# Performance work log

Hardware: AMD Instinct MI355X
Metric: run time of the kernel (lower is better)

Reference implementation:

```python
import jax, jax.numpy as jnp
import numpy as np

D_MODEL = 1024
OMEGA_DIM = 64
VQ_CODES = 256
VQ_DIM = 64
N_PARAMS = OMEGA_DIM * (OMEGA_DIM - 1) // 2  # 2016
TRIU_R, TRIU_C = np.triu_indices(OMEGA_DIM, k=1)
RMS_EPS = 1e-6
NORM_EPS = 1e-12  # F.normalize default


def setup_inputs() -> dict:
    key = jax.random.key(0)
    ks = jax.random.split(key, 12)
    B, L = 16, 4096
    s = 0.02
    return {
        "x": jax.random.normal(ks[0], (B, L, D_MODEL), jnp.float32),
        "omega_proj_w": jax.random.normal(ks[1], (N_PARAMS, D_MODEL), jnp.float32) * s,
        "omega_proj_b": jnp.zeros((N_PARAMS,), jnp.float32),
        "omega_out_w": jax.random.normal(ks[2], (D_MODEL, OMEGA_DIM), jnp.float32) * s,
        "omega_out_b": jnp.zeros((D_MODEL,), jnp.float32),
        "vq_proj_in_w": jax.random.normal(ks[3], (VQ_DIM, D_MODEL), jnp.float32) * s,
        "vq_proj_in_b": jnp.zeros((VQ_DIM,), jnp.float32),
        "vq_proj_out_w": jax.random.normal(ks[4], (D_MODEL, VQ_DIM), jnp.float32) * s,
        "vq_proj_out_b": jnp.zeros((D_MODEL,), jnp.float32),
        "codebook": jax.random.normal(ks[5], (VQ_CODES, VQ_DIM), jnp.float32),
        "omega_mix": jnp.float32(0.1),
        "vq_mix": jnp.float32(0.05),
        "norm_w": jnp.ones((D_MODEL,), jnp.float32),
    }


def _normalize(v):
    n = jnp.linalg.norm(v, axis=-1, keepdims=True)
    return v / jnp.maximum(n, NORM_EPS)


def _rmsnorm(x, w):
    ms = jnp.mean(x * x, axis=-1, keepdims=True)
    return x * jax.lax.rsqrt(ms + RMS_EPS) * w


def reference(x, omega_proj_w, omega_proj_b, omega_out_w, omega_out_b,
              vq_proj_in_w, vq_proj_in_b, vq_proj_out_w, vq_proj_out_b,
              codebook, omega_mix, vq_mix, norm_w):
    B = x.shape[0]
    residual = x
    h_mean = jnp.mean(x, axis=1)  # [B, d_model]

    # --- Lie branch: skew-symmetric Omega -> Cayley (3rd-order Neumann) ---
    params = h_mean @ omega_proj_w.T + omega_proj_b  # [B, n_params]
    omega = jnp.zeros((B, OMEGA_DIM, OMEGA_DIM), x.dtype).at[:, TRIU_R, TRIU_C].set(params)
    omega = omega - jnp.swapaxes(omega, -1, -2)
    I = jnp.eye(OMEGA_DIM, dtype=x.dtype)
    omega2 = jnp.einsum('bij,bjk->bik', omega, omega)
    omega3 = jnp.einsum('bij,bjk->bik', omega2, omega)
    G = I + omega + 0.5 * omega2 + (1.0 / 6.0) * omega3  # [B, n, n]

    x_head = x[:, :, :OMEGA_DIM]
    x_rotated = jnp.einsum('bld,bde->ble', x_head, G)
    lie_out = x_rotated @ omega_out_w.T + omega_out_b  # [B, L, d_model]

    # --- VQ branch: cosine-sim codebook lookup with straight-through ---
    vq_input = h_mean @ vq_proj_in_w.T + vq_proj_in_b  # [B, vq_dim]
    scores = _normalize(vq_input) @ _normalize(codebook).T  # [B, vq_codes]
    vq_idx = jnp.argmax(scores, axis=-1)
    vq_code = codebook[vq_idx]  # [B, vq_dim]
    vq_out = vq_input + jax.lax.stop_gradient(vq_code - vq_input)
    vq_contribution = (vq_out @ vq_proj_out_w.T + vq_proj_out_b)[:, None, :]  # [B,1,d_model]

    out = residual + omega_mix * lie_out + vq_mix * vq_contribution
    return _rmsnorm(out, norm_w)
```

## Files before the change

### kernel.cpp

```cpp
#include <hip/hip_runtime.h>
#include <hip/hip_bf16.h>
#include <math.h>

#define BB 16
#define LL 4096
#define DD 1024
#define OD 64
#define NP 2016
#define NC 256
#define VD 64
#define NCHUNK 64
#define LCH (LL / NCHUNK)
#define TT 16
#define TPB 256
#define NROW (NP + VD)

typedef __attribute__((ext_vector_type(8))) short bf16x8;
typedef __attribute__((ext_vector_type(4))) float f32x4;

__device__ __forceinline__ int triu_idx(int r, int c) {
  return r * 63 - (r * (r - 1)) / 2 + (c - r - 1);
}

__device__ __forceinline__ unsigned short f2bf(float f) {
  unsigned int u = __float_as_uint(f);
  u += 0x7fffu + ((u >> 16) & 1u);
  return (unsigned short)(u >> 16);
}

__global__ void k_partial(const float* __restrict__ x, float* __restrict__ partial) {
  const int b = blockIdx.y, ch = blockIdx.x, tid = threadIdx.x;
  const float4* xp = (const float4*)(x + ((size_t)b * LL + (size_t)ch * LCH) * DD) + tid;
  float4 s = make_float4(0.f, 0.f, 0.f, 0.f);
  #pragma unroll 8
  for (int l = 0; l < LCH; ++l) {
    float4 v = xp[(size_t)l * (DD / 4)];
    s.x += v.x; s.y += v.y; s.z += v.z; s.w += v.w;
  }
  ((float4*)(partial + ((size_t)(b * NCHUNK + ch)) * DD))[tid] = s;
}

__global__ void k_mean(const float* __restrict__ partial, float* __restrict__ hm) {
  const int b = blockIdx.x, tid = threadIdx.x;
  float4 s = make_float4(0.f, 0.f, 0.f, 0.f);
  for (int c = 0; c < NCHUNK; ++c) {
    float4 v = ((const float4*)(partial + ((size_t)(b * NCHUNK + c)) * DD))[tid];
    s.x += v.x; s.y += v.y; s.z += v.z; s.w += v.w;
  }
  const float inv = 1.0f / (float)LL;
  s.x *= inv; s.y *= inv; s.z *= inv; s.w *= inv;
  ((float4*)(hm + (size_t)b * DD))[tid] = s;
}

__global__ void k_params(const float* __restrict__ hm,
                         const float* __restrict__ opw, const float* __restrict__ opb,
                         const float* __restrict__ viw, const float* __restrict__ vib,
                         float* __restrict__ params, float* __restrict__ vqi_g) {
  const int wave = threadIdx.x >> 6, lane = threadIdx.x & 63;
  const int p = blockIdx.x * 4 + wave;
  if (p >= NROW) return;
  const bool isvq = (p >= NP);
  const float* wr = isvq ? (viw + (size_t)(p - NP) * DD) : (opw + (size_t)p * DD);
  float acc[BB];
  #pragma unroll
  for (int b = 0; b < BB; ++b) acc[b] = 0.f;
  for (int i = 0; i < DD; i += 64) {
    const float wv = wr[i + lane];
    #pragma unroll
    for (int b = 0; b < BB; ++b) acc[b] = fmaf(wv, hm[b * DD + i + lane], acc[b]);
  }
  const float bias = isvq ? vib[p - NP] : opb[p];
  #pragma unroll
  for (int b = 0; b < BB; ++b) {
    float v = acc[b];
    #pragma unroll
    for (int mk = 32; mk; mk >>= 1) v += __shfl_xor(v, mk, 64);
    if (lane == 0) {
      if (isvq) vqi_g[(size_t)b * VD + (p - NP)] = v + bias;
      else      params[(size_t)b * NP + p] = v + bias;
    }
  }
}

__global__ void k_perb(const float* __restrict__ params, const float* __restrict__ vqi_g,
                       const float* __restrict__ cb,
                       const float* __restrict__ oob, const float* __restrict__ vow,
                       const float* __restrict__ vob,
                       const float* __restrict__ omix_p, const float* __restrict__ vmix_p,
                       float* __restrict__ Gout, float* __restrict__ cvec) {
  const int b = blockIdx.x, tid = threadIdx.x;
  __shared__ float om[OD][OD + 1];
  __shared__ float om2[OD][OD + 1];
  __shared__ float vqi[VD];
  __shared__ float sc[NC];
  __shared__ int si[NC];
  __shared__ float cd[VD];
  __shared__ float nv_s;
  const float* par = params + (size_t)b * NP;

  if (tid < VD) vqi[tid] = vqi_g[(size_t)b * VD + tid];
  for (int e2 = tid; e2 < OD * OD; e2 += 256) {
    int i = e2 >> 6, j = e2 & 63;
    float v = 0.f;
    if (i < j) v = par[triu_idx(i, j)];
    else if (i > j) v = -par[triu_idx(j, i)];
    om[i][j] = v;
  }
  __syncthreads();
  if (tid == 0) {
    float s = 0.f;
    for (int k = 0; k < VD; ++k) s += vqi[k] * vqi[k];
    nv_s = fmaxf(sqrtf(s), 1e-12f);
  }
  for (int e2 = tid; e2 < OD * OD; e2 += 256) {
    int i = e2 >> 6, j = e2 & 63;
    float s = 0.f;
    #pragma unroll 8
    for (int k = 0; k < OD; ++k) s = fmaf(om[i][k], om[k][j], s);
    om2[i][j] = s;
  }
  __syncthreads();
  for (int e2 = tid; e2 < OD * OD; e2 += 256) {
    int i = e2 >> 6, j = e2 & 63;
    float s3 = 0.f;
    #pragma unroll 8
    for (int k = 0; k < OD; ++k) s3 = fmaf(om2[i][k], om[k][j], s3);
    float gv = om[i][j] + 0.5f * om2[i][j] + (1.f / 6.f) * s3 + (i == j ? 1.f : 0.f);
    Gout[(size_t)b * OD * OD + e2] = gv;
  }
  {
    const float* cr = cb + (size_t)tid * VD;
    float dot = 0.f, ssq = 0.f;
    #pragma unroll 8
    for (int k = 0; k < VD; ++k) { float cvv = cr[k]; dot = fmaf(cvv, vqi[k], dot); ssq = fmaf(cvv, cvv, ssq); }
    float ncn = fmaxf(sqrtf(ssq), 1e-12f);
    sc[tid] = dot / (nv_s * ncn);
    si[tid] = tid;
  }
  __syncthreads();
  for (int s = 128; s > 0; s >>= 1) {
    if (tid < s) {
      float a = sc[tid], b2 = sc[tid + s];
      int ia = si[tid], ib = si[tid + s];
      if (b2 > a || (b2 == a && ib < ia)) { sc[tid] = b2; si[tid] = ib; }
    }
    __syncthreads();
  }
  const int best = si[0];
  if (tid < VD) cd[tid] = cb[(size_t)best * VD + tid];
  __syncthreads();
  const float omix = omix_p[0], vmix = vmix_p[0];
  for (int e = tid; e < DD; e += 256) {
    float a = vob[e];
    const float* wr = vow + (size_t)e * VD;
    #pragma unroll 8
    for (int k = 0; k < VD; ++k) a = fmaf(cd[k], wr[k], a);
    cvec[(size_t)b * DD + e] = fmaf(omix, oob[e], vmix * a);
  }
}

__global__ void k_MTB(const float* __restrict__ G, const float* __restrict__ oow,
                      const float* __restrict__ omix_p, unsigned short* __restrict__ MTB) {
  const int b = blockIdx.y, eb = blockIdx.x * 64, tid = threadIdx.x;
  __shared__ float g[OD][OD + 1];
  __shared__ float wl[64][65];
  for (int e2 = tid; e2 < OD * OD; e2 += 256) g[e2 >> 6][e2 & 63] = G[(size_t)b * OD * OD + e2];
  for (int e2 = tid; e2 < 64 * 64; e2 += 256) wl[e2 >> 6][e2 & 63] = oow[(size_t)(eb + (e2 >> 6)) * 64 + (e2 & 63)];
  __syncthreads();
  const float omix = omix_p[0];
  for (int o = tid; o < 4096; o += 256) {
    int el = o >> 6, d = o & 63;
    float s = 0.f;
    #pragma unroll
    for (int k = 0; k < 64; ++k) s = fmaf(g[d][k], wl[el][k], s);
    MTB[((size_t)b * DD + eb + el) * OD + d] = f2bf(omix * s);
  }
}

#define STAGE_XH(BUF, TTOK)                                                          \
  if (stager) {                                                                      \
    const float4 v = *(const float4*)(x + xrow + (size_t)((TTOK) + stok) * DD + sd0);\
    unsigned int lo = (unsigned int)f2bf(v.x) | ((unsigned int)f2bf(v.y) << 16);     \
    unsigned int hi = (unsigned int)f2bf(v.z) | ((unsigned int)f2bf(v.w) << 16);     \
    *(uint2*)((char*)&(BUF)[0][0] + stok * 144 + sd0 * 2) = make_uint2(lo, hi);      \
  }

#define LOAD_RES(DST, TTOK)                                                          \
  _Pragma("unroll")                                                                  \
  for (int et = 0; et < 4; ++et) {                                                   \
    _Pragma("unroll")                                                                \
    for (int r = 0; r < 4; ++r)                                                      \
      DST[et][r] = x[xrow + (size_t)((TTOK) + g * 4 + r) * DD + ebase + et * 16 + c];\
  }

#define COMPUTE_TILE(XBUF, RES, PAR, TTOK)                                           \
  {                                                                                  \
    const char* xbB = (const char*)&(XBUF)[0][0];                                    \
    bf16x8 af0 = *(const bf16x8*)(xbB + c * 144 + 0 * 64 + g * 16);                  \
    bf16x8 af1 = *(const bf16x8*)(xbB + c * 144 + 1 * 64 + g * 16);                  \
    f32x4 acc[4];                                                                    \
    _Pragma("unroll")                                                                \
    for (int et = 0; et < 4; ++et) {                                                 \
      acc[et] = (f32x4){0.f, 0.f, 0.f, 0.f};                                         \
      acc[et] = __builtin_amdgcn_mfma_f32_16x16x32_bf16(af0, bf[et][0], acc[et], 0, 0, 0); \
      acc[et] = __builtin_amdgcn_mfma_f32_16x16x32_bf16(af1, bf[et][1], acc[et], 0, 0, 0); \
    }                                                                                \
    float p[4] = {0.f, 0.f, 0.f, 0.f};                                               \
    _Pragma("unroll")                                                                \
    for (int et = 0; et < 4; ++et) {                                                 \
      _Pragma("unroll")                                                              \
      for (int r = 0; r < 4; ++r) {                                                  \
        const float y = RES[et][r] + acc[et][r] + ce_r[et];                          \
        acc[et][r] = y;                                                              \
        p[r] = fmaf(y, y, p[r]);                                                     \
      }                                                                              \
    }                                                                                \
    _Pragma("unroll")                                                                \
    for (int mk = 1; mk < 16; mk <<= 1) {                                            \
      _Pragma("unroll")                                                              \
      for (int r = 0; r < 4; ++r) p[r] += __shfl_xor(p[r], mk, 64);                  \
    }                                                                                \
    if (c == 0) {                                                                    \
      _Pragma("unroll")                                                              \
      for (int r = 0; r < 4; ++r) red[PAR][g * 4 + r][w] = p[r];                     \
    }                                                                                \
    __syncthreads();                                                                 \
    float sc_r[4];                                                                   \
    _Pragma("unroll")                                                                \
    for (int r = 0; r < 4; ++r) {                                                    \
      const float4* rp = (const float4*)&red[PAR][g * 4 + r][0];                     \
      const float4 s0 = rp[0], s1 = rp[1], s2 = rp[2], s3 = rp[3];                   \
      const float s = s0.x + s0.y + s0.z + s0.w + s1.x + s1.y + s1.z + s1.w          \
                    + s2.x + s2.y + s2.z + s2.w + s3.x + s3.y + s3.z + s3.w;         \
      sc_r[r] = rsqrtf(s * (1.f / (float)DD) + 1e-6f);                               \
    }                                                                                \
    _Pragma("unroll")                                                                \
    for (int et = 0; et < 4; ++et) {                                                 \
      _Pragma("unroll")                                                              \
      for (int r = 0; r < 4; ++r) {                                                  \
        out[xrow + (size_t)((TTOK) + g * 4 + r) * DD + ebase + et * 16 + c] =        \
            acc[et][r] * sc_r[r] * nw_r[et];                                         \
      }                                                                              \
    }                                                                                \
  }

__global__ __launch_bounds__(1024)
void k_mfma(const float* __restrict__ x, const unsigned short* __restrict__ MTB,
            const float* __restrict__ cvec, const float* __restrict__ nw,
            float* __restrict__ out) {
  const int b = blockIdx.y;
  const int Tblk = blockIdx.x * TPB;
  const int tid = threadIdx.x;
  const int w = tid >> 6, lane = tid & 63;
  const int c = lane & 15, g = lane >> 4;
  const int ebase = w * 64;

  __shared__ unsigned short xh[2][TT][72];
  __shared__ float red[2][TT][20];

  bf16x8 bf[4][2];
  {
    const unsigned short* mp = MTB + ((size_t)b * DD + ebase + c) * OD + g * 8;
    #pragma unroll
    for (int et = 0; et < 4; ++et) {
      #pragma unroll
      for (int ks = 0; ks < 2; ++ks)
        bf[et][ks] = *(const bf16x8*)(mp + (size_t)et * 16 * OD + ks * 32);
    }
  }
  float ce_r[4], nw_r[4];
  #pragma unroll
  for (int et = 0; et < 4; ++et) {
    ce_r[et] = cvec[(size_t)b * DD + ebase + et * 16 + c];
    nw_r[et] = nw[ebase + et * 16 + c];
  }

  const size_t xrow = ((size_t)b * LL + Tblk) * DD;
  const int stok = tid >> 4, sd0 = (tid & 15) * 4;
  const bool stager = (tid < 256);

  float resA[4][4], resB[4][4];

  STAGE_XH(xh[0], 0)
  LOAD_RES(resA, 0)
  __syncthreads();

  #pragma unroll 1
  for (int it = 0; it < TPB / (2 * TT); ++it) {
    const int te = it * 2 * TT;
    const int to = te + TT;
    const int tn = te + 2 * TT;
    STAGE_XH(xh[1], to)
    LOAD_RES(resB, to)
    COMPUTE_TILE(xh[0], resA, 0, te)
    if (it + 1 < TPB / (2 * TT)) {
      STAGE_XH(xh[0], tn)
      LOAD_RES(resA, tn)
    }
    COMPUTE_TILE(xh[1], resB, 1, to)
  }
}

extern "C" void kernel_launch(void* const* d_in, const int* in_sizes, int n_in,
                              void* d_out, int out_size, void* d_ws, size_t ws_size,
                              hipStream_t stream) {
  (void)in_sizes; (void)n_in; (void)out_size; (void)ws_size;
  const float* x    = (const float*)d_in[0];
  const float* opw  = (const float*)d_in[1];
  const float* opb  = (const float*)d_in[2];
  const float* oow  = (const float*)d_in[3];
  const float* oob  = (const float*)d_in[4];
  const float* viw  = (const float*)d_in[5];
  const float* vib  = (const float*)d_in[6];
  const float* vow  = (const float*)d_in[7];
  const float* vob  = (const float*)d_in[8];
  const float* cb   = (const float*)d_in[9];
  const float* omix = (const float*)d_in[10];
  const float* vmix = (const float*)d_in[11];
  const float* nw   = (const float*)d_in[12];
  float* out = (float*)d_out;

  float* ws      = (float*)d_ws;
  float* partial = ws;
  float* hm      = ws + 1048576;
  float* params  = ws + 1064960;
  float* vqi_g   = ws + 1097216;
  float* G       = ws + 1098240;
  unsigned short* MTB = (unsigned short*)(ws + 1163776);
  float* cvec    = ws + 1688064;

  k_partial<<<dim3(NCHUNK, BB), 256, 0, stream>>>(x, partial);
  k_mean<<<BB, 256, 0, stream>>>(partial, hm);
  k_params<<<NROW / 4, 256, 0, stream>>>(hm, opw, opb, viw, vib, params, vqi_g);
  k_perb<<<BB, 256, 0, stream>>>(params, vqi_g, cb, oob, vow, vob, omix, vmix, G, cvec);
  k_MTB<<<dim3(16, BB), 256, 0, stream>>>(G, oow, omix, MTB);
  k_mfma<<<dim3(LL / TPB, BB), 1024, 0, stream>>>(x, MTB, cvec, nw, out);
}
```

Before: 252.3 us.

## Fuse all six stages into one persistent kernel with grid barriers

Merges the mean reduction, parameter GEMV, Cayley/VQ per-batch work, MTB build and the MFMA main pass into one 256-block persistent kernel. Stages are separated by atomic-counter grid barriers, and the counters are reset with a memset before each launch. The G matrix is no longer written to global memory: each block recomputes G for its batch in shared memory before forming its slice of MTB. This removes five launch gaps and the small-grid serial stages. The risks are deadlock if all 256 blocks of 1024 threads are not co-resident, the cost of redundant G computation, and lower parallelism in the reduction stages.

```diff
diff --git a/kernel.cpp b/kernel.cpp
--- a/kernel.cpp
+++ b/kernel.cpp
@@ -9,11 +9,10 @@
 #define NP 2016
 #define NC 256
 #define VD 64
-#define NCHUNK 64
-#define LCH (LL / NCHUNK)
 #define TT 16
 #define TPB 256
 #define NROW (NP + VD)
+#define NBLK 256
 
 typedef __attribute__((ext_vector_type(8))) short bf16x8;
 typedef __attribute__((ext_vector_type(4))) float f32x4;
@@ -21,283 +20,297 @@
 __device__ __forceinline__ int triu_idx(int r, int c) {
   return r * 63 - (r * (r - 1)) / 2 + (c - r - 1);
 }
-
 __device__ __forceinline__ unsigned short f2bf(float f) {
   unsigned int u = __float_as_uint(f);
   u += 0x7fffu + ((u >> 16) & 1u);
   return (unsigned short)(u >> 16);
 }
 
-__global__ void k_partial(const float* __restrict__ x, float* __restrict__ partial) {
-  const int b = blockIdx.y, ch = blockIdx.x, tid = threadIdx.x;
-  const float4* xp = (const float4*)(x + ((size_t)b * LL + (size_t)ch * LCH) * DD) + tid;
-  float4 s = make_float4(0.f, 0.f, 0.f, 0.f);
-  #pragma unroll 8
-  for (int l = 0; l < LCH; ++l) {
-    float4 v = xp[(size_t)l * (DD / 4)];
-    s.x += v.x; s.y += v.y; s.z += v.z; s.w += v.w;
-  }
-  ((float4*)(partial + ((size_t)(b * NCHUNK + ch)) * DD))[tid] = s;
-}
-
-__global__ void k_mean(const float* __restrict__ partial, float* __restrict__ hm) {
-  const int b = blockIdx.x, tid = threadIdx.x;
-  float4 s = make_float4(0.f, 0.f, 0.f, 0.f);
-  for (int c = 0; c < NCHUNK; ++c) {
-    float4 v = ((const float4*)(partial + ((size_t)(b * NCHUNK + c)) * DD))[tid];
-    s.x += v.x; s.y += v.y; s.z += v.z; s.w += v.w;
-  }
-  const float inv = 1.0f / (float)LL;
-  s.x *= inv; s.y *= inv; s.z *= inv; s.w *= inv;
-  ((float4*)(hm + (size_t)b * DD))[tid] = s;
-}
-
-__global__ void k_params(const float* __restrict__ hm,
-                         const float* __restrict__ opw, const float* __restrict__ opb,
-                         const float* __restrict__ viw, const float* __restrict__ vib,
-                         float* __restrict__ params, float* __restrict__ vqi_g) {
-  const int wave = threadIdx.x >> 6, lane = threadIdx.x & 63;
-  const int p = blockIdx.x * 4 + wave;
-  if (p >= NROW) return;
-  const bool isvq = (p >= NP);
-  const float* wr = isvq ? (viw + (size_t)(p - NP) * DD) : (opw + (size_t)p * DD);
-  float acc[BB];
-  #pragma unroll
-  for (int b = 0; b < BB; ++b) acc[b] = 0.f;
-  for (int i = 0; i < DD; i += 64) {
-    const float wv = wr[i + lane];
+__device__ __forceinline__ void gbar(unsigned int* cnt) {
+  __syncthreads();
+  __threadfence();
+  if (threadIdx.x == 0) {
+    atomicAdd(cnt, 1u);
+    while (atomicAdd(cnt, 0u) < NBLK) __builtin_amdgcn_s_sleep(2);
+  }
+  __syncthreads();
+  __threadfence();
+}
+
+__global__ __launch_bounds__(1024)
+void k_mega(const float* __restrict__ x,
+            const float* __restrict__ opw, const float* __restrict__ opb,
+            const float* __restrict__ oow, const float* __restrict__ oob,
+            const float* __restrict__ viw, const float* __restrict__ vib,
+            const float* __restrict__ vow, const float* __restrict__ vob,
+            const float* __restrict__ cb,
+            const float* __restrict__ omix_p, const float* __restrict__ vmix_p,
+            const float* __restrict__ nw,
+            float* __restrict__ partial2, float* __restrict__ hm,
+            float* __restrict__ params, float* __restrict__ vqi_g,
+            unsigned short* __restrict__ MTB, float* __restrict__ cvec,
+            unsigned int* cnt, float* __restrict__ out) {
+  const int bid = blockIdx.x, tid = threadIdx.x;
+  __shared__ __align__(16) char smem[49920];
+
+  {
+    const int b = bid >> 4, seg = bid & 15;
+    const int c4 = tid & 255, toff = tid >> 8;
+    const float4* xp = (const float4*)(x + ((size_t)b * LL + seg * 256 + toff) * DD) + c4;
+    float4 s = make_float4(0.f, 0.f, 0.f, 0.f);
+    #pragma unroll 8
+    for (int l = 0; l < 64; ++l) {
+      float4 v = xp[(size_t)l * DD];
+      s.x += v.x; s.y += v.y; s.z += v.z; s.w += v.w;
+    }
+    ((float4*)(partial2 + (size_t)(bid * 4 + toff) * DD))[c4] = s;
+  }
+  gbar(cnt + 0);
+
+  if (bid < BB) {
+    float s = 0.f;
+    const float* pr = partial2 + (size_t)bid * 64 * DD + tid;
+    #pragma unroll 8
+    for (int r2 = 0; r2 < 64; ++r2) s += pr[(size_t)r2 * DD];
+    hm[(size_t)bid * DD + tid] = s * (1.f / (float)LL);
+  }
+  gbar(cnt + 1);
+
+  {
+    const int w = tid >> 6, lane = tid & 63;
+    const int p = bid * 16 + w;
+    if (p < NROW) {
+      const bool isvq = (p >= NP);
+      const float* wr = isvq ? (viw + (size_t)(p - NP) * DD) : (opw + (size_t)p * DD);
+      float acc[BB];
+      #pragma unroll
+      for (int b = 0; b < BB; ++b) acc[b] = 0.f;
+      for (int i = 0; i < DD; i += 64) {
+        const float wv = wr[i + lane];
+        #pragma unroll
+        for (int b = 0; b < BB; ++b) acc[b] = fmaf(wv, hm[b * DD + i + lane], acc[b]);
+      }
+      const float bias = isvq ? vib[p - NP] : opb[p];
+      #pragma unroll
+      for (int b = 0; b < BB; ++b) {
+        float v = acc[b];
+        #pragma unroll
+        for (int mk = 32; mk; mk >>= 1) v += __shfl_xor(v, mk, 64);
+        if (lane == 0) {
+          if (isvq) vqi_g[(size_t)b * VD + (p - NP)] = v + bias;
+          else      params[(size_t)b * NP + p] = v + bias;
+        }
+      }
+    }
+  }
+  gbar(cnt + 2);
+
+  {
+    const int b = bid >> 4, chunk = bid & 15, eb = chunk * 64;
+    float (*om)[OD + 1]  = (float(*)[OD + 1])(smem);
+    float (*om2)[OD + 1] = (float(*)[OD + 1])(smem + 16640);
+    float (*gs)[OD + 1]  = (float(*)[OD + 1])(smem + 33280);
+    const float* par = params + (size_t)b * NP;
+    const float omix = omix_p[0];
+
+    for (int e2 = tid; e2 < OD * OD; e2 += 1024) {
+      int i = e2 >> 6, j = e2 & 63;
+      float v = 0.f;
+      if (i < j) v = par[triu_idx(i, j)];
+      else if (i > j) v = -par[triu_idx(j, i)];
+      om[i][j] = v;
+    }
+    __syncthreads();
+    for (int e2 = tid; e2 < OD * OD; e2 += 1024) {
+      int i = e2 >> 6, j = e2 & 63;
+      float s = 0.f;
+      #pragma unroll 8
+      for (int k = 0; k < OD; ++k) s = fmaf(om[i][k], om[k][j], s);
+      om2[i][j] = s;
+    }
+    __syncthreads();
+    for (int e2 = tid; e2 < OD * OD; e2 += 1024) {
+      int i = e2 >> 6, j = e2 & 63;
+      float s3 = 0.f;
+      #pragma unroll 8
+      for (int k = 0; k < OD; ++k) s3 = fmaf(om2[i][k], om[k][j], s3);
+      gs[i][j] = om[i][j] + 0.5f * om2[i][j] + (1.f / 6.f) * s3 + (i == j ? 1.f : 0.f);
+    }
+    __syncthreads();
+    float (*wl)[OD + 1] = (float(*)[OD + 1])(smem);
+    for (int e2 = tid; e2 < 64 * 64; e2 += 1024)
+      wl[e2 >> 6][e2 & 63] = oow[(size_t)(eb + (e2 >> 6)) * 64 + (e2 & 63)];
+    __syncthreads();
+    for (int o = tid; o < 4096; o += 1024) {
+      int el = o >> 6, d = o & 63;
+      float s = 0.f;
+      #pragma unroll
+      for (int k = 0; k < 64; ++k) s = fmaf(gs[d][k], wl[el][k], s);
+      MTB[((size_t)b * DD + eb + el) * OD + d] = f2bf(omix * s);
+    }
+    if (chunk == 0) {
+      float* vq  = (float*)(smem + 16640);
+      float* scb = (float*)(smem + 16640 + 256);
+      int*   sib = (int*)  (smem + 16640 + 1280);
+      float* cd  = (float*)(smem + 16640 + 2304);
+      float* nvp = (float*)(smem + 16640 + 2560);
+      if (tid < VD) vq[tid] = vqi_g[(size_t)b * VD + tid];
+      __syncthreads();
+      if (tid == 0) {
+        float s = 0.f;
+        for (int k = 0; k < VD; ++k) s += vq[k] * vq[k];
+        nvp[0] = fmaxf(sqrtf(s), 1e-12f);
+      }
+      __syncthreads();
+      if (tid < NC) {
+        const float* cr = cb + (size_t)tid * VD;
+        float dot = 0.f, ssq = 0.f;
+        #pragma unroll 8
+        for (int k = 0; k < VD; ++k) { float cv = cr[k]; dot = fmaf(cv, vq[k], dot); ssq = fmaf(cv, cv, ssq); }
+        scb[tid] = dot / (nvp[0] * fmaxf(sqrtf(ssq), 1e-12f));
+        sib[tid] = tid;
+      }
+      __syncthreads();
+      for (int s2 = 128; s2 > 0; s2 >>= 1) {
+        if (tid < s2) {
+          float a = scb[tid], b2 = scb[tid + s2];
+          int ia = sib[tid], ib = sib[tid + s2];
+          if (b2 > a || (b2 == a && ib < ia)) { scb[tid] = b2; sib[tid] = ib; }
+        }
+        __syncthreads();
+      }
+      const int best = sib[0];
+      if (tid < VD) cd[tid] = cb[(size_t)best * VD + tid];
+      __syncthreads();
+      const float vmix = vmix_p[0];
+      {
+        const int e = tid;
+        float a = vob[e];
+        const float* wr2 = vow + (size_t)e * VD;
+        #pragma unroll 8
+        for (int k = 0; k < VD; ++k) a = fmaf(cd[k], wr2[k], a);
+        cvec[(size_t)b * DD + e] = fmaf(omix, oob[e], vmix * a);
+      }
+    }
+  }
+  gbar(cnt + 3);
+
+  {
+    const int b = bid >> 4;
+    const int Tblk = (bid & 15) * TPB;
+    const int w = tid >> 6, lane = tid & 63;
+    const int c = lane & 15, g = lane >> 4;
+    const int ebase = w * 64;
+
+#define XB(q) ((char*)smem + (q) * 2304)
+#define RB(q) ((char*)smem + 4608 + (q) * 1280)
+
+    bf16x8 bf[4][2];
+    {
+      const unsigned short* mp = MTB + ((size_t)b * DD + ebase + c) * OD + g * 8;
+      #pragma unroll
+      for (int et = 0; et < 4; ++et) {
+        #pragma unroll
+        for (int ks = 0; ks < 2; ++ks)
+          bf[et][ks] = *(const bf16x8*)(mp + (size_t)et * 16 * OD + ks * 32);
+      }
+    }
+    float ce_r[4], nw_r[4];
     #pragma unroll
-    for (int b = 0; b < BB; ++b) acc[b] = fmaf(wv, hm[b * DD + i + lane], acc[b]);
-  }
-  const float bias = isvq ? vib[p - NP] : opb[p];
-  #pragma unroll
-  for (int b = 0; b < BB; ++b) {
-    float v = acc[b];
-    #pragma unroll
-    for (int mk = 32; mk; mk >>= 1) v += __shfl_xor(v, mk, 64);
-    if (lane == 0) {
-      if (isvq) vqi_g[(size_t)b * VD + (p - NP)] = v + bias;
-      else      params[(size_t)b * NP + p] = v + bias;
-    }
-  }
-}
-
-__global__ void k_perb(const float* __restrict__ params, const float* __restrict__ vqi_g,
-                       const float* __restrict__ cb,
-                       const float* __restrict__ oob, const float* __restrict__ vow,
-                       const float* __restrict__ vob,
-                       const float* __restrict__ omix_p, const float* __restrict__ vmix_p,
-                       float* __restrict__ Gout, float* __restrict__ cvec) {
-  const int b = blockIdx.x, tid = threadIdx.x;
-  __shared__ float om[OD][OD + 1];
-  __shared__ float om2[OD][OD + 1];
-  __shared__ float vqi[VD];
-  __shared__ float sc[NC];
-  __shared__ int si[NC];
-  __shared__ float cd[VD];
-  __shared__ float nv_s;
-  const float* par = params + (size_t)b * NP;
-
-  if (tid < VD) vqi[tid] = vqi_g[(size_t)b * VD + tid];
-  for (int e2 = tid; e2 < OD * OD; e2 += 256) {
-    int i = e2 >> 6, j = e2 & 63;
-    float v = 0.f;
-    if (i < j) v = par[triu_idx(i, j)];
-    else if (i > j) v = -par[triu_idx(j, i)];
-    om[i][j] = v;
-  }
-  __syncthreads();
-  if (tid == 0) {
-    float s = 0.f;
-    for (int k = 0; k < VD; ++k) s += vqi[k] * vqi[k];
-    nv_s = fmaxf(sqrtf(s), 1e-12f);
-  }
-  for (int e2 = tid; e2 < OD * OD; e2 += 256) {
-    int i = e2 >> 6, j = e2 & 63;
-    float s = 0.f;
-    #pragma unroll 8
-    for (int k = 0; k < OD; ++k) s = fmaf(om[i][k], om[k][j], s);
-    om2[i][j] = s;
-  }
-  __syncthreads();
-  for (int e2 = tid; e2 < OD * OD; e2 += 256) {
-    int i = e2 >> 6, j = e2 & 63;
-    float s3 = 0.f;
-    #pragma unroll 8
-    for (int k = 0; k < OD; ++k) s3 = fmaf(om2[i][k], om[k][j], s3);
-    float gv = om[i][j] + 0.5f * om2[i][j] + (1.f / 6.f) * s3 + (i == j ? 1.f : 0.f);
-    Gout[(size_t)b * OD * OD + e2] = gv;
-  }
-  {
-    const float* cr = cb + (size_t)tid * VD;
-    float dot = 0.f, ssq = 0.f;
-    #pragma unroll 8
-    for (int k = 0; k < VD; ++k) { float cvv = cr[k]; dot = fmaf(cvv, vqi[k], dot); ssq = fmaf(cvv, cvv, ssq); }
-    float ncn = fmaxf(sqrtf(ssq), 1e-12f);
-    sc[tid] = dot / (nv_s * ncn);
-    si[tid] = tid;
-  }
-  __syncthreads();
-  for (int s = 128; s > 0; s >>= 1) {
-    if (tid < s) {
-      float a = sc[tid], b2 = sc[tid + s];
-      int ia = si[tid], ib = si[tid + s];
-      if (b2 > a || (b2 == a && ib < ia)) { sc[tid] = b2; si[tid] = ib; }
-    }
-    __syncthreads();
-  }
-  const int best = si[0];
-  if (tid < VD) cd[tid] = cb[(size_t)best * VD + tid];
-  __syncthreads();
-  const float omix = omix_p[0], vmix = vmix_p[0];
-  for (int e = tid; e < DD; e += 256) {
-    float a = vob[e];
-    const float* wr = vow + (size_t)e * VD;
-    #pragma unroll 8
-    for (int k = 0; k < VD; ++k) a = fmaf(cd[k], wr[k], a);
-    cvec[(size_t)b * DD + e] = fmaf(omix, oob[e], vmix * a);
-  }
-}
-
-__global__ void k_MTB(const float* __restrict__ G, const float* __restrict__ oow,
-                      const float* __restrict__ omix_p, unsigned short* __restrict__ MTB) {
-  const int b = blockIdx.y, eb = blockIdx.x * 64, tid = threadIdx.x;
-  __shared__ float g[OD][OD + 1];
-  __shared__ float wl[64][65];
-  for (int e2 = tid; e2 < OD * OD; e2 += 256) g[e2 >> 6][e2 & 63] = G[(size_t)b * OD * OD + e2];
-  for (int e2 = tid; e2 < 64 * 64; e2 += 256) wl[e2 >> 6][e2 & 63] = oow[(size_t)(eb + (e2 >> 6)) * 64 + (e2 & 63)];
-  __syncthreads();
-  const float omix = omix_p[0];
-  for (int o = tid; o < 4096; o += 256) {
-    int el = o >> 6, d = o & 63;
-    float s = 0.f;
-    #pragma unroll
-    for (int k = 0; k < 64; ++k) s = fmaf(g[d][k], wl[el][k], s);
-    MTB[((size_t)b * DD + eb + el) * OD + d] = f2bf(omix * s);
-  }
-}
-
-#define STAGE_XH(BUF, TTOK)                                                          \
-  if (stager) {                                                                      \
-    const float4 v = *(const float4*)(x + xrow + (size_t)((TTOK) + stok) * DD + sd0);\
-    unsigned int lo = (unsigned int)f2bf(v.x) | ((unsigned int)f2bf(v.y) << 16);     \
-    unsigned int hi = (unsigned int)f2bf(v.z) | ((unsigned int)f2bf(v.w) << 16);     \
-    *(uint2*)((char*)&(BUF)[0][0] + stok * 144 + sd0 * 2) = make_uint2(lo, hi);      \
-  }
+    for (int et = 0; et < 4; ++et) {
+      ce_r[et] = cvec[(size_t)b * DD + ebase + et * 16 + c];
+      nw_r[et] = nw[ebase + et * 16 + c];
+    }
+
+    const size_t xrow = ((size_t)b * LL + Tblk) * DD;
+    const int stok = tid >> 4, sd0 = (tid & 15) * 4;
+    const bool stager = (tid < 256);
+    float resA[4][4], resB[4][4];
+
+#define STAGE_XH(Q, TTOK)                                                            \
+    if (stager) {                                                                    \
+      const float4 v = *(const float4*)(x + xrow + (size_t)((TTOK) + stok) * DD + sd0); \
+      unsigned int lo = (unsigned int)f2bf(v.x) | ((unsigned int)f2bf(v.y) << 16);   \
+      unsigned int hi = (unsigned int)f2bf(v.z) | ((unsigned int)f2bf(v.w) << 16);   \
+      *(uint2*)(XB(Q) + stok * 144 + sd0 * 2) = make_uint2(lo, hi);                  \
+    }
 
 #define LOAD_RES(DST, TTOK)                                                          \
-  _Pragma("unroll")                                                                  \
-  for (int et = 0; et < 4; ++et) {                                                   \
-    _Pragma("unroll")                                                                \
-    for (int r = 0; r < 4; ++r)                                                      \
-      DST[et][r] = x[xrow + (size_t)((TTOK) + g * 4 + r) * DD + ebase + et * 16 + c];\
-  }
-
-#define COMPUTE_TILE(XBUF, RES, PAR, TTOK)                                           \
-  {                                                                                  \
-    const char* xbB = (const char*)&(XBUF)[0][0];                                    \
-    bf16x8 af0 = *(const bf16x8*)(xbB + c * 144 + 0 * 64 + g * 16);                  \
-    bf16x8 af1 = *(const bf16x8*)(xbB + c * 144 + 1 * 64 + g * 16);                  \
-    f32x4 acc[4];                                                                    \
     _Pragma("unroll")                                                                \
     for (int et = 0; et < 4; ++et) {                                                 \
-      acc[et] = (f32x4){0.f, 0.f, 0.f, 0.f};                                         \
-      acc[et] = __builtin_amdgcn_mfma_f32_16x16x32_bf16(af0, bf[et][0], acc[et], 0, 0, 0); \
-      acc[et] = __builtin_amdgcn_mfma_f32_16x16x32_bf16(af1, bf[et][1], acc[et], 0, 0, 0); \
-    }                                                                                \
-    float p[4] = {0.f, 0.f, 0.f, 0.f};                                               \
-    _Pragma("unroll")                                                                \
-    for (int et = 0; et < 4; ++et) {                                                 \
+      _Pragma("unroll")                                                              \
+      for (int r = 0; r < 4; ++r)                                                    \
+        DST[et][r] = x[xrow + (size_t)((TTOK) + g * 4 + r) * DD + ebase + et * 16 + c]; \
+    }
+
+#define COMPUTE_TILE(Q, RES, PB, TTOK)                                               \
+    {                                                                                \
+      bf16x8 af0 = *(const bf16x8*)(XB(Q) + c * 144 + g * 16);                       \
+      bf16x8 af1 = *(const bf16x8*)(XB(Q) + c * 144 + 64 + g * 16);                  \
+      f32x4 acc[4];                                                                  \
+      _Pragma("unroll")                                                              \
+      for (int et = 0; et < 4; ++et) {                                               \
+        acc[et] = (f32x4){0.f, 0.f, 0.f, 0.f};                                       \
+        acc[et] = __builtin_amdgcn_mfma_f32_16x16x32_bf16(af0, bf[et][0], acc[et], 0, 0, 0); \
+        acc[et] = __builtin_amdgcn_mfma_f32_16x16x32_bf16(af1, bf[et][1], acc[et], 0, 0, 0); \
+      }                                                                              \
+      float pp[4] = {0.f, 0.f, 0.f, 0.f};                                            \
+      _Pragma("unroll")                                                              \
+      for (int et = 0; et < 4; ++et) {                                               \
+        _Pragma("unroll")                                                            \
+        for (int r = 0; r < 4; ++r) {                                                \
+          const float y = RES[et][r] + acc[et][r] + ce_r[et];                        \
+          acc[et][r] = y;                                                            \
+          pp[r] = fmaf(y, y, pp[r]);                                                 \
+        }                                                                            \
+      }                                                                              \
+      _Pragma("unroll")                                                              \
+      for (int mk = 1; mk < 16; mk <<= 1) {                                          \
+        _Pragma("unroll")                                                            \
+        for (int r = 0; r < 4; ++r) pp[r] += __shfl_xor(pp[r], mk, 64);              \
+      }                                                                              \
+      if (c == 0) {                                                                  \
+        _Pragma("unroll")                                                            \
+        for (int r = 0; r < 4; ++r) *(float*)(RB(PB) + (g * 4 + r) * 80 + w * 4) = pp[r]; \
+      }                                                                              \
+      __syncthreads();                                                               \
+      float sc_r[4];                                                                 \
       _Pragma("unroll")                                                              \
       for (int r = 0; r < 4; ++r) {                                                  \
-        const float y = RES[et][r] + acc[et][r] + ce_r[et];                          \
-        acc[et][r] = y;                                                              \
-        p[r] = fmaf(y, y, p[r]);                                                     \
-      }                                                                              \
-    }                                                                                \
-    _Pragma("unroll")                                                                \
-    for (int mk = 1; mk < 16; mk <<= 1) {                                            \
-      _Pragma("unroll")                                                              \
-      for (int r = 0; r < 4; ++r) p[r] += __shfl_xor(p[r], mk, 64);                  \
-    }                                                                                \
-    if (c == 0) {                                                                    \
-      _Pragma("unroll")                                                              \
-      for (int r = 0; r < 4; ++r) red[PAR][g * 4 + r][w] = p[r];                     \
-    }                                                                                \
-    __syncthreads();                                                                 \
-    float sc_r[4];                                                                   \
-    _Pragma("unroll")                                                                \
-    for (int r = 0; r < 4; ++r) {                                                    \
-      const float4* rp = (const float4*)&red[PAR][g * 4 + r][0];                     \
-      const float4 s0 = rp[0], s1 = rp[1], s2 = rp[2], s3 = rp[3];                   \
-      const float s = s0.x + s0.y + s0.z + s0.w + s1.x + s1.y + s1.z + s1.w          \
-                    + s2.x + s2.y + s2.z + s2.w + s3.x + s3.y + s3.z + s3.w;         \
-      sc_r[r] = rsqrtf(s * (1.f / (float)DD) + 1e-6f);                               \
-    }                                                                                \
-    _Pragma("unroll")                                                                \
-    for (int et = 0; et < 4; ++et) {                                                 \
-      _Pragma("unroll")                                                              \
-      for (int r = 0; r < 4; ++r) {                                                  \
-        out[xrow + (size_t)((TTOK) + g * 4 + r) * DD + ebase + et * 16 + c] =        \
-            acc[et][r] * sc_r[r] * nw_r[et];                                         \
-      }                                                                              \
-    }                                                                                \
-  }
-
-__global__ __launch_bounds__(1024)
-void k_mfma(const float* __restrict__ x, const unsigned short* __restrict__ MTB,
-            const float* __restrict__ cvec, const float* __restrict__ nw,
-            float* __restrict__ out) {
-  const int b = blockIdx.y;
-  const int Tblk = blockIdx.x * TPB;
-  const int tid = threadIdx.x;
-  const int w = tid >> 6, lane = tid & 63;
-  const int c = lane & 15, g = lane >> 4;
-  const int ebase = w * 64;
-
-  __shared__ unsigned short xh[2][TT][72];
-  __shared__ float red[2][TT][20];
-
-  bf16x8 bf[4][2];
-  {
-    const unsigned short* mp = MTB + ((size_t)b * DD + ebase + c) * OD + g * 8;
-    #pragma unroll
-    for (int et = 0; et < 4; ++et) {
-      #pragma unroll
-      for (int ks = 0; ks < 2; ++ks)
-        bf[et][ks] = *(const bf16x8*)(mp + (size_t)et * 16 * OD + ks * 32);
-    }
-  }
-  float ce_r[4], nw_r[4];
-  #pragma unroll
-  for (int et = 0; et < 4; ++et) {
-    ce_r[et] = cvec[(size_t)b * DD + ebase + et * 16 + c];
-    nw_r[et] = nw[ebase + et * 16 + c];
-  }
-
-  const size_t xrow = ((size_t)b * LL + Tblk) * DD;
-  const int stok = tid >> 4, sd0 = (tid & 15) * 4;
-  const bool stager = (tid < 256);
-
-  float resA[4][4], resB[4][4];
-
-  STAGE_XH(xh[0], 0)
-  LOAD_RES(resA, 0)
-  __syncthreads();
-
-  #pragma unroll 1
-  for (int it = 0; it < TPB / (2 * TT); ++it) {
-    const int te = it * 2 * TT;
-    const int to = te + TT;
-    const int tn = te + 2 * TT;
-    STAGE_XH(xh[1], to)
-    LOAD_RES(resB, to)
-    COMPUTE_TILE(xh[0], resA, 0, te)
-    if (it + 1 < TPB / (2 * TT)) {
-      STAGE_XH(xh[0], tn)
-      LOAD_RES(resA, tn)
-    }
-    COMPUTE_TILE(xh[1], resB, 1, to)
+        const float4* rp = (const float4*)(RB(PB) + (g * 4 + r) * 80);               \
+        const float4 s0 = rp[0], s1 = rp[1], s2 = rp[2], s3 = rp[3];                 \
+        const float s = s0.x + s0.y + s0.z + s0.w + s1.x + s1.y + s1.z + s1.w        \
+                      + s2.x + s2.y + s2.z + s2.w + s3.x + s3.y + s3.z + s3.w;       \
+        sc_r[r] = rsqrtf(s * (1.f / (float)DD) + 1e-6f);                             \
+      }                                                                              \
+      _Pragma("unroll")                                                              \
+      for (int et = 0; et < 4; ++et) {                                               \
+        _Pragma("unroll")                                                            \
+        for (int r = 0; r < 4; ++r) {                                                \
+          out[xrow + (size_t)((TTOK) + g * 4 + r) * DD + ebase + et * 16 + c] =      \
+              acc[et][r] * sc_r[r] * nw_r[et];                                       \
+        }                                                                            \
+      }                                                                              \
+    }
+
+    STAGE_XH(0, 0)
+    LOAD_RES(resA, 0)
+    __syncthreads();
+
+    #pragma unroll 1
+    for (int it = 0; it < TPB / (2 * TT); ++it) {
+      const int te = it * 2 * TT;
+      const int to = te + TT;
+      const int tn = te + 2 * TT;
+      STAGE_XH(1, to)
+      LOAD_RES(resB, to)
+      COMPUTE_TILE(0, resA, 0, te)
+      if (it + 1 < TPB / (2 * TT)) {
+        STAGE_XH(0, tn)
+        LOAD_RES(resA, tn)
+      }
+      COMPUTE_TILE(1, resB, 1, to)
+    }
   }
 }
 
@@ -320,19 +333,18 @@
   const float* nw   = (const float*)d_in[12];
   float* out = (float*)d_out;
 
-  float* ws      = (float*)d_ws;
-  float* partial = ws;
-  float* hm      = ws + 1048576;
-  float* params  = ws + 1064960;
-  float* vqi_g   = ws + 1097216;
-  float* G       = ws + 1098240;
-  unsigned short* MTB = (unsigned short*)(ws + 1163776);
-  float* cvec    = ws + 1688064;
-
-  k_partial<<<dim3(NCHUNK, BB), 256, 0, stream>>>(x, partial);
-  k_mean<<<BB, 256, 0, stream>>>(partial, hm);
-  k_params<<<NROW / 4, 256, 0, stream>>>(hm, opw, opb, viw, vib, params, vqi_g);
-  k_perb<<<BB, 256, 0, stream>>>(params, vqi_g, cb, oob, vow, vob, omix, vmix, G, cvec);
-  k_MTB<<<dim3(16, BB), 256, 0, stream>>>(G, oow, omix, MTB);
-  k_mfma<<<dim3(LL / TPB, BB), 1024, 0, stream>>>(x, MTB, cvec, nw, out);
-}
+  float* ws       = (float*)d_ws;
+  float* partial2 = ws;
+  float* hm       = ws + 1048576;
+  float* params   = ws + 1064960;
+  float* vqi_g    = ws + 1097216;
+  unsigned short* MTB = (unsigned short*)(ws + 1098240);
+  float* cvec     = ws + 1622528;
+  unsigned int* cnt = (unsigned int*)(ws + 1638912);
+
+  hipMemsetAsync(cnt, 0, 32, stream);
+  k_mega<<<NBLK, 1024, 0, stream>>>(x, opw, opb, oow, oob, viw, vib, vow, vob,
+                                    cb, omix, vmix, nw,
+                                    partial2, hm, params, vqi_g, MTB, cvec,
+                                    cnt, out);
+}
```

Result: slower. 827.9 us (+228.2%).
